# Optimization experiments

Measured on AMD Instinct MI355X. Metric: run time of the kernel, lower is better.

The kernel has to match this reference:

```python
import jax, jax.numpy as jnp
import numpy as np

B, T, H, K = 64, 512, 768, 4  # batch, seq_len, bert hidden, tagset (BMES)


def setup_inputs() -> dict:
    key = jax.random.key(0)
    ks = jax.random.split(key, 6)
    return {
        "sentences": jax.random.normal(ks[0], (B, T, H), dtype=jnp.float32),
        "W": jax.random.normal(ks[1], (K, H), dtype=jnp.float32) * (1.0 / np.sqrt(H)),
        "b": jax.random.normal(ks[2], (K,), dtype=jnp.float32) * 0.01,
        "start_transitions": jax.random.uniform(ks[3], (K,), dtype=jnp.float32, minval=-0.1, maxval=0.1),
        "end_transitions": jax.random.uniform(ks[4], (K,), dtype=jnp.float32, minval=-0.1, maxval=0.1),
        "transitions": jax.random.uniform(ks[5], (K, K), dtype=jnp.float32, minval=-0.1, maxval=0.1),
    }


def reference(sentences, W, b, start_transitions, end_transitions, transitions):
    # hidden2tag linear projection: [B,T,H] @ [H,K] -> emissions [B,T,K]
    emissions = jnp.einsum("bth,kh->btk", sentences, W) + b

    # Viterbi forward pass (torchcrf decode with full mask)
    score0 = start_transitions + emissions[:, 0]  # [B,K]

    def step(score, emit_t):
        # score[b,i] + transitions[i,j] -> [B,K_prev,K_next]
        cand = score[:, :, None] + transitions[None, :, :]
        bp = jnp.argmax(cand, axis=1)            # [B,K] backpointer to prev tag
        new_score = jnp.max(cand, axis=1) + emit_t
        return new_score, bp

    emits_t = jnp.swapaxes(emissions[:, 1:], 0, 1)  # [T-1,B,K]
    last_score, history = jax.lax.scan(step, score0, emits_t)

    final = last_score + end_transitions            # [B,K]
    best_last = jnp.argmax(final, axis=-1)          # [B]

    # Backtrack: path[t] = history[t][b, path[t+1]] for t = T-2 .. 0
    def back(tag, bp_t):
        prev = jnp.take_along_axis(bp_t, tag[:, None], axis=1)[:, 0]
        return prev, prev

    _, prev_tags = jax.lax.scan(back, best_last, history, reverse=True)  # [T-1,B]
    tags = jnp.concatenate([prev_tags, best_last[None, :]], axis=0)      # [T,B]
    return jnp.transpose(tags).astype(jnp.int32)                         # [B,T]
```

## Files before the change

kernel.cpp:

```cpp
#include <hip/hip_runtime.h>
#include <stdint.h>

#define BB 64
#define TT 512
#define HH 768
#define KK 4

__global__ __launch_bounds__(256) void emis_kernel(
    const float* __restrict__ sent, const float* __restrict__ W,
    const float* __restrict__ bias, float* __restrict__ emis) {
  const int lane  = threadIdx.x & 63;
  const int wave  = threadIdx.x >> 6;
  const int gwave = blockIdx.x * 4 + wave;
  const int k     = lane & 3;
  const int slice = lane >> 2;

  const float4* Wv = (const float4*)W;
  float4 w[12];
#pragma unroll
  for (int u = 0; u < 12; ++u) w[u] = Wv[k * 192 + slice * 12 + u];
  const float bk = bias[k];

#pragma unroll
  for (int i = 0; i < 4; ++i) {
    const int row = gwave + 8192 * i;
    const float4* sv = (const float4*)(sent + (size_t)row * HH);
    float a = 0.f;
#pragma unroll
    for (int u = 0; u < 12; ++u) {
      float4 x = sv[slice * 12 + u];
      a = fmaf(x.x, w[u].x, a);
      a = fmaf(x.y, w[u].y, a);
      a = fmaf(x.z, w[u].z, a);
      a = fmaf(x.w, w[u].w, a);
    }
    a += __shfl_xor(a, 4);
    a += __shfl_xor(a, 8);
    a += __shfl_xor(a, 16);
    a += __shfl_xor(a, 32);
    if (lane < 4) emis[row * 4 + k] = a + bk;
  }
}

template <int CTRL>
__device__ __forceinline__ float qperm(float x) {
  return __int_as_float(__builtin_amdgcn_update_dpp(
      0, __float_as_int(x), CTRL, 0xF, 0xF, true));
}

__device__ __forceinline__ uint32_t map_compose(uint32_t f, uint32_t g) {
  uint32_t h = 0;
#pragma unroll
  for (int x = 0; x < 4; ++x) {
    uint32_t gx = (g >> (2 * x)) & 3u;
    uint32_t fx = (f >> (2 * gx)) & 3u;
    h |= fx << (2 * x);
  }
  return h;
}

__global__ __launch_bounds__(64) void viterbi_kernel(
    const float* __restrict__ emis, const float* __restrict__ trans,
    const float* __restrict__ startT, const float* __restrict__ endT,
    int* __restrict__ out) {
  const int b    = blockIdx.x;
  const int lane = threadIdx.x;
  const int j    = lane & 3;

  __shared__ uint8_t bp[4][520];

  const int i1 = (j + 1) & 3, i2 = (j + 2) & 3, i3 = (j + 3) & 3;
  const float tr0 = trans[j * 4 + j];
  const float tr1 = trans[i1 * 4 + j];
  const float tr2 = trans[i2 * 4 + j];
  const float tr3 = trans[i3 * 4 + j];

  const float* eb = emis + b * (TT * KK);
  float s = startT[j] + eb[j];

  auto step = [&](int t, float e) {
    float s1 = qperm<0x39>(s);
    float s2 = qperm<0x4E>(s);
    float s3 = qperm<0x93>(s);
    float c0 = s + tr0;
    float c1 = s1 + tr1;
    float c2 = s2 + tr2;
    float c3 = s3 + tr3;
    float m = c0; int bi = j;
    if (c1 > m) { m = c1; bi = i1; }
    if (c2 > m) { m = c2; bi = i2; }
    if (c3 > m) { m = c3; bi = i3; }
    s = m + e;
    if (lane < 4) bp[j][t] = (uint8_t)bi;
  };

  float ebuf[8];
#pragma unroll
  for (int q = 0; q < 8; ++q) ebuf[q] = eb[(1 + q) * 4 + j];

  for (int c = 0; c < 63; ++c) {
    float enext[8];
    const int base = 8 * c + 9;
#pragma unroll
    for (int q = 0; q < 8; ++q) {
      int tt = base + q; if (tt > 511) tt = 511;
      enext[q] = eb[tt * 4 + j];
    }
#pragma unroll
    for (int q = 0; q < 8; ++q) step(8 * c + 1 + q, ebuf[q]);
#pragma unroll
    for (int q = 0; q < 8; ++q) ebuf[q] = enext[q];
  }
#pragma unroll
  for (int q = 0; q < 7; ++q) step(505 + q, ebuf[q]);

  float f = s + endT[j];
  {
    float f1 = qperm<0x39>(f);
    float f2 = qperm<0x4E>(f);
    float f3 = qperm<0x93>(f);
    float m = f; int bi = j;
    if (f1 > m) { m = f1; bi = i1; }
    if (f2 > m) { m = f2; bi = i2; }
    if (f3 > m) { m = f3; bi = i3; }
    f = (float)bi;
  }
  const int best_last = (int)f;

  __syncthreads();

  const int lo = 8 * lane + 1;
  uint32_t g[8];
  uint32_t A = 0xE4;
#pragma unroll
  for (int q = 7; q >= 0; --q) {
    const int sq = lo + q;
    uint32_t mq = 0xE4;
    if (sq <= 511) {
      mq = (uint32_t)bp[0][sq] | ((uint32_t)bp[1][sq] << 2) |
           ((uint32_t)bp[2][sq] << 4) | ((uint32_t)bp[3][sq] << 6);
    }
    g[q] = mq;
    A = map_compose(mq, A);
  }

  uint32_t V = A;
#pragma unroll
  for (int d = 1; d < 64; d <<= 1) {
    uint32_t o = __shfl_down(V, d);
    if (lane + d < 64) V = map_compose(V, o);
  }
  uint32_t S = __shfl_down(V, 1);
  if (lane == 63) S = 0xE4;

  int cur = (int)((S >> (2 * best_last)) & 3u);
  const int hi = min(lo + 7, 511);
  int* ob = out + b * TT;
  ob[hi] = cur;
#pragma unroll
  for (int q = 7; q >= 0; --q) {
    const int sq = lo + q;
    if (sq <= 511) {
      cur = (int)((g[q] >> (2 * cur)) & 3u);
      ob[sq - 1] = cur;
    }
  }
}

extern "C" void kernel_launch(void* const* d_in, const int* in_sizes, int n_in,
                              void* d_out, int out_size, void* d_ws, size_t ws_size,
                              hipStream_t stream) {
  const float* sent   = (const float*)d_in[0];
  const float* W      = (const float*)d_in[1];
  const float* bias   = (const float*)d_in[2];
  const float* startT = (const float*)d_in[3];
  const float* endT   = (const float*)d_in[4];
  const float* trans  = (const float*)d_in[5];
  float* emis = (float*)d_ws;
  int* outp   = (int*)d_out;

  emis_kernel<<<2048, 256, 0, stream>>>(sent, W, bias, emis);
  viterbi_kernel<<<BB, 64, 0, stream>>>(emis, trans, startT, endT, outp);
}
```

Before: 205.8 us.

## Store Viterbi scores and recompute backpointers in parallel; restructure emission GEMV

The Viterbi forward loop now saves only the per-step scores to shared memory, using DPP broadcasts and fmax without tracking argmax. The backpointers are recomputed in parallel during the backtrack phase, which shortens the serial dependency chain. The emission kernel is restructured so each wave computes all four tags for 8 rows: W stays in registers, the next row is prefetched, the reduction uses DPP plus two shuffles, and the grid is halved. Recomputing the argmax has to reproduce the forward max exactly, which it does because it uses the same float adds, and it adds parallel work in the backtrack.

```diff
diff --git a/kernel.cpp b/kernel.cpp
--- a/kernel.cpp
+++ b/kernel.cpp
@@ -5,6 +5,12 @@
 #define TT 512
 #define HH 768
 #define KK 4
+
+template <int CTRL>
+__device__ __forceinline__ float dppf(float x) {
+  return __int_as_float(__builtin_amdgcn_update_dpp(
+      0, __float_as_int(x), CTRL, 0xF, 0xF, true));
+}
 
 __global__ __launch_bounds__(256) void emis_kernel(
     const float* __restrict__ sent, const float* __restrict__ W,
@@ -12,41 +18,61 @@
   const int lane  = threadIdx.x & 63;
   const int wave  = threadIdx.x >> 6;
   const int gwave = blockIdx.x * 4 + wave;
-  const int k     = lane & 3;
-  const int slice = lane >> 2;
 
   const float4* Wv = (const float4*)W;
-  float4 w[12];
-#pragma unroll
-  for (int u = 0; u < 12; ++u) w[u] = Wv[k * 192 + slice * 12 + u];
-  const float bk = bias[k];
-
-#pragma unroll
-  for (int i = 0; i < 4; ++i) {
-    const int row = gwave + 8192 * i;
-    const float4* sv = (const float4*)(sent + (size_t)row * HH);
-    float a = 0.f;
-#pragma unroll
-    for (int u = 0; u < 12; ++u) {
-      float4 x = sv[slice * 12 + u];
-      a = fmaf(x.x, w[u].x, a);
-      a = fmaf(x.y, w[u].y, a);
-      a = fmaf(x.z, w[u].z, a);
-      a = fmaf(x.w, w[u].w, a);
-    }
-    a += __shfl_xor(a, 4);
-    a += __shfl_xor(a, 8);
-    a += __shfl_xor(a, 16);
-    a += __shfl_xor(a, 32);
-    if (lane < 4) emis[row * 4 + k] = a + bk;
-  }
-}
-
-template <int CTRL>
-__device__ __forceinline__ float qperm(float x) {
-  return __int_as_float(__builtin_amdgcn_update_dpp(
-      0, __float_as_int(x), CTRL, 0xF, 0xF, true));
-}
+  float4 w[4][3];
+#pragma unroll
+  for (int k = 0; k < 4; ++k)
+#pragma unroll
+    for (int c = 0; c < 3; ++c) w[k][c] = Wv[k * 192 + c * 64 + lane];
+
+  const float4 bb = ((const float4*)bias)[0];
+  const float4* sv = (const float4*)sent;
+
+  int row = gwave * 8;
+  float4 x[3];
+#pragma unroll
+  for (int c = 0; c < 3; ++c) x[c] = sv[(size_t)row * 192 + c * 64 + lane];
+
+#pragma unroll
+  for (int it = 0; it < 8; ++it) {
+    float4 xn[3];
+    if (it < 7) {
+#pragma unroll
+      for (int c = 0; c < 3; ++c)
+        xn[c] = sv[(size_t)(row + 1) * 192 + c * 64 + lane];
+    }
+    float a0 = 0.f, a1 = 0.f, a2 = 0.f, a3 = 0.f;
+#pragma unroll
+    for (int c = 0; c < 3; ++c) {
+      a0 = fmaf(x[c].x, w[0][c].x, a0); a0 = fmaf(x[c].y, w[0][c].y, a0);
+      a0 = fmaf(x[c].z, w[0][c].z, a0); a0 = fmaf(x[c].w, w[0][c].w, a0);
+      a1 = fmaf(x[c].x, w[1][c].x, a1); a1 = fmaf(x[c].y, w[1][c].y, a1);
+      a1 = fmaf(x[c].z, w[1][c].z, a1); a1 = fmaf(x[c].w, w[1][c].w, a1);
+      a2 = fmaf(x[c].x, w[2][c].x, a2); a2 = fmaf(x[c].y, w[2][c].y, a2);
+      a2 = fmaf(x[c].z, w[2][c].z, a2); a2 = fmaf(x[c].w, w[2][c].w, a2);
+      a3 = fmaf(x[c].x, w[3][c].x, a3); a3 = fmaf(x[c].y, w[3][c].y, a3);
+      a3 = fmaf(x[c].z, w[3][c].z, a3); a3 = fmaf(x[c].w, w[3][c].w, a3);
+    }
+#define RED16(a)                                                   \
+    a += dppf<0x124>(a); a += dppf<0x128>(a);                      \
+    a += dppf<0xB1>(a);  a += dppf<0x4E>(a);
+    RED16(a0) RED16(a1) RED16(a2) RED16(a3)
+#undef RED16
+    a0 += __shfl_xor(a0, 16); a0 += __shfl_xor(a0, 32);
+    a1 += __shfl_xor(a1, 16); a1 += __shfl_xor(a1, 32);
+    a2 += __shfl_xor(a2, 16); a2 += __shfl_xor(a2, 32);
+    a3 += __shfl_xor(a3, 16); a3 += __shfl_xor(a3, 32);
+    if (lane == 0) {
+      float4 o; o.x = a0 + bb.x; o.y = a1 + bb.y; o.z = a2 + bb.z; o.w = a3 + bb.w;
+      ((float4*)emis)[row] = o;
+    }
+    row += 1;
+#pragma unroll
+    for (int c = 0; c < 3; ++c) x[c] = xn[c];
+  }
+}
+
 
 __device__ __forceinline__ uint32_t map_compose(uint32_t f, uint32_t g) {
   uint32_t h = 0;
@@ -67,31 +93,29 @@
   const int lane = threadIdx.x;
   const int j    = lane & 3;
 
-  __shared__ uint8_t bp[4][520];
-
-  const int i1 = (j + 1) & 3, i2 = (j + 2) & 3, i3 = (j + 3) & 3;
-  const float tr0 = trans[j * 4 + j];
-  const float tr1 = trans[i1 * 4 + j];
-  const float tr2 = trans[i2 * 4 + j];
-  const float tr3 = trans[i3 * 4 + j];
+  __shared__ float sc[TT][4];
+
+  const float tr0 = trans[0 * 4 + j];
+  const float tr1 = trans[1 * 4 + j];
+  const float tr2 = trans[2 * 4 + j];
+  const float tr3 = trans[3 * 4 + j];
 
   const float* eb = emis + b * (TT * KK);
   float s = startT[j] + eb[j];
+  if (lane < 4) sc[0][j] = s;
 
   auto step = [&](int t, float e) {
-    float s1 = qperm<0x39>(s);
-    float s2 = qperm<0x4E>(s);
-    float s3 = qperm<0x93>(s);
-    float c0 = s + tr0;
-    float c1 = s1 + tr1;
-    float c2 = s2 + tr2;
-    float c3 = s3 + tr3;
-    float m = c0; int bi = j;
-    if (c1 > m) { m = c1; bi = i1; }
-    if (c2 > m) { m = c2; bi = i2; }
-    if (c3 > m) { m = c3; bi = i3; }
+    float v0 = dppf<0x00>(s);
+    float v1 = dppf<0x55>(s);
+    float v2 = dppf<0xAA>(s);
+    float v3 = dppf<0xFF>(s);
+    float c0 = v0 + tr0;
+    float c1 = v1 + tr1;
+    float c2 = v2 + tr2;
+    float c3 = v3 + tr3;
+    float m = fmaxf(fmaxf(c0, c1), fmaxf(c2, c3));
     s = m + e;
-    if (lane < 4) bp[j][t] = (uint8_t)bi;
+    if (lane < 4) sc[t][j] = s;
   };
 
   float ebuf[8];
@@ -115,19 +139,24 @@
   for (int q = 0; q < 7; ++q) step(505 + q, ebuf[q]);
 
   float f = s + endT[j];
+  int best_last;
   {
-    float f1 = qperm<0x39>(f);
-    float f2 = qperm<0x4E>(f);
-    float f3 = qperm<0x93>(f);
-    float m = f; int bi = j;
-    if (f1 > m) { m = f1; bi = i1; }
-    if (f2 > m) { m = f2; bi = i2; }
-    if (f3 > m) { m = f3; bi = i3; }
-    f = (float)bi;
-  }
-  const int best_last = (int)f;
+    float f0 = dppf<0x00>(f);
+    float f1 = dppf<0x55>(f);
+    float f2 = dppf<0xAA>(f);
+    float f3 = dppf<0xFF>(f);
+    float bm = f0; int bi = 0;
+    if (f1 > bm) { bm = f1; bi = 1; }
+    if (f2 > bm) { bm = f2; bi = 2; }
+    if (f3 > bm) { bm = f3; bi = 3; }
+    best_last = bi;
+  }
 
   __syncthreads();
+
+  float t16[16];
+#pragma unroll
+  for (int i = 0; i < 16; ++i) t16[i] = trans[i];
 
   const int lo = 8 * lane + 1;
   uint32_t g[8];
@@ -137,8 +166,20 @@
     const int sq = lo + q;
     uint32_t mq = 0xE4;
     if (sq <= 511) {
-      mq = (uint32_t)bp[0][sq] | ((uint32_t)bp[1][sq] << 2) |
-           ((uint32_t)bp[2][sq] << 4) | ((uint32_t)bp[3][sq] << 6);
+      const float4 pv = *((const float4*)sc[sq - 1]);
+      mq = 0;
+#pragma unroll
+      for (int j2 = 0; j2 < 4; ++j2) {
+        float c0 = pv.x + t16[0 * 4 + j2];
+        float c1 = pv.y + t16[1 * 4 + j2];
+        float c2 = pv.z + t16[2 * 4 + j2];
+        float c3 = pv.w + t16[3 * 4 + j2];
+        float bm = c0; uint32_t bi = 0;
+        if (c1 > bm) { bm = c1; bi = 1; }
+        if (c2 > bm) { bm = c2; bi = 2; }
+        if (c3 > bm) { bm = c3; bi = 3; }
+        mq |= bi << (2 * j2);
+      }
     }
     g[q] = mq;
     A = map_compose(mq, A);
@@ -179,6 +220,6 @@
   float* emis = (float*)d_ws;
   int* outp   = (int*)d_out;
 
-  emis_kernel<<<2048, 256, 0, stream>>>(sent, W, bias, emis);
+  emis_kernel<<<1024, 256, 0, stream>>>(sent, W, bias, emis);
   viterbi_kernel<<<BB, 64, 0, stream>>>(emis, trans, startT, endT, outp);
 }
```

Result: faster. 175.4 us (-14.8%).
